# Performance work log

Hardware: AMD Instinct MI355X
Metric: run time of the kernel (lower is better)

## Reference

```python
import jax, jax.numpy as jnp
import numpy as np

D_K = 64
SCALE = 1.0 / np.sqrt(D_K).astype(np.float32)


def setup_inputs() -> dict:
    key = jax.random.key(0)
    kq, kk, kv = jax.random.split(key, 3)
    B, S, D = 4, 2048, 512
    q = jax.random.normal(kq, (B, S, D), dtype=jnp.float32)
    k = jax.random.normal(kk, (B, S, D), dtype=jnp.float32)
    v = jax.random.normal(kv, (B, S, D), dtype=jnp.float32)
    return {"q": q, "k": k, "v": v}


def reference(q, k, v):
    # n_head == 1: the per-head strided slices are the full tensors.
    # Original computes BOTH 'new_k' (scaled q@k^T) and 'new_v' (unscaled q@k^T);
    # note: v is never used in the original forward math (faithful reproduction).
    qk = jnp.einsum('bsd,btd->bst', q, k)           # [B, S, S]
    scores = qk * SCALE                              # new_k
    attn = jax.nn.softmax(scores, axis=2)            # softmax over dim 2
    # dropout with p=0.1 is identity in eval / deterministic reference
    out = jnp.matmul(attn, qk)                       # attn @ new_v -> [B, S, S]
    return out
```

## Files before the change

### kernel.cpp

```cpp
#include <hip/hip_runtime.h>
#include <hip/hip_bf16.h>
#include <stdint.h>


#define SS 2048
#define DD 512
#define BATCH 4
#define NT 32

typedef __attribute__((ext_vector_type(8))) short short8;
typedef __attribute__((ext_vector_type(8))) _Float16 half8;
typedef __attribute__((ext_vector_type(4))) float floatx4;
typedef __attribute__((ext_vector_type(4))) float float4v;
typedef __attribute__((ext_vector_type(4))) unsigned int uintx4;

#define GLOBAL_AS const __attribute__((address_space(1)))
#define LDS_AS __attribute__((address_space(3)))

__device__ __forceinline__ float bf2f(uint32_t hbits) {
    union { uint32_t u; float f; } c; c.u = hbits << 16; return c.f;
}
__device__ __forceinline__ uint32_t f2bf_rne(float f) {
    union { float f; uint32_t u; } c; c.f = f;
    return (c.u + 0x7fffu + ((c.u >> 16) & 1u)) >> 16;
}
__device__ __forceinline__ uint32_t pk2h(float x, float y) {
    _Float16 hx = (_Float16)x, hy = (_Float16)y;
    union { _Float16 h; uint16_t u; } cx, cy;
    cx.h = hx; cy.h = hy;
    return (uint32_t)cx.u | ((uint32_t)cy.u << 16);
}

union PackU { uint32_t u[4]; short8 s8; };

__global__ __launch_bounds__(256, 2) void gemm1_kernel(
    const float* __restrict__ Q, const float* __restrict__ K,
    uint16_t* __restrict__ qk, uint16_t* __restrict__ qkT)
{
    const int b  = blockIdx.z;
    const int s0 = blockIdx.y * 128;
    const int t0 = blockIdx.x * 128;
    const float* qb = Q + (size_t)b * SS * DD;
    const float* kb = K + (size_t)b * SS * DD;

    __shared__ uint16_t Ah[2 * 128 * 32];
    __shared__ uint16_t Bh[2 * 128 * 32];

    const int tid  = threadIdx.x;
    const int lane = tid & 63;
    const int wave = tid >> 6;
    const int wm   = wave >> 1;
    const int wn   = wave & 1;
    const int fm   = lane & 15;
    const int quad = lane >> 4;

    floatx4 acc[4][4];
#pragma unroll
    for (int i = 0; i < 4; ++i)
#pragma unroll
        for (int j = 0; j < 4; ++j)
            acc[i][j] = (floatx4)0.0f;

    const int r  = tid >> 1;
    const int c0 = (tid & 1) * 16;
    const float* gA = qb + (size_t)(s0 + r) * DD + c0;
    const float* gB = kb + (size_t)(t0 + r) * DD + c0;

    for (int k0 = 0; k0 < DD; k0 += 64) {
        uint32_t pa[2][8], pb[2][8];
#pragma unroll
        for (int ks = 0; ks < 2; ++ks) {
            float4v a4[4], b4[4];
#pragma unroll
            for (int l = 0; l < 4; ++l) {
                a4[l] = *(const float4v*)(gA + k0 + ks * 32 + l * 4);
                b4[l] = *(const float4v*)(gB + k0 + ks * 32 + l * 4);
            }
#pragma unroll
            for (int l = 0; l < 4; ++l) {
                pa[ks][2 * l]     = pk2h(a4[l][0], a4[l][1]);
                pa[ks][2 * l + 1] = pk2h(a4[l][2], a4[l][3]);
                pb[ks][2 * l]     = pk2h(b4[l][0], b4[l][1]);
                pb[ks][2 * l + 1] = pk2h(b4[l][2], b4[l][3]);
            }
        }
        __syncthreads();
#pragma unroll
        for (int ks = 0; ks < 2; ++ks) {
            PackU p;
            p.u[0]=pa[ks][0]; p.u[1]=pa[ks][1]; p.u[2]=pa[ks][2]; p.u[3]=pa[ks][3];
            *(short8*)(&Ah[ks * 4096 + r * 32 + c0]) = p.s8;
            p.u[0]=pa[ks][4]; p.u[1]=pa[ks][5]; p.u[2]=pa[ks][6]; p.u[3]=pa[ks][7];
            *(short8*)(&Ah[ks * 4096 + r * 32 + c0 + 8]) = p.s8;
            p.u[0]=pb[ks][0]; p.u[1]=pb[ks][1]; p.u[2]=pb[ks][2]; p.u[3]=pb[ks][3];
            *(short8*)(&Bh[ks * 4096 + r * 32 + c0]) = p.s8;
            p.u[0]=pb[ks][4]; p.u[1]=pb[ks][5]; p.u[2]=pb[ks][6]; p.u[7==7?7:7]=pb[ks][7];
            p.u[0]=pb[ks][4]; p.u[1]=pb[ks][5]; p.u[2]=pb[ks][6]; p.u[3]=pb[ks][7];
            *(short8*)(&Bh[ks * 4096 + r * 32 + c0 + 8]) = p.s8;
        }
        __syncthreads();

#pragma unroll
        for (int ks = 0; ks < 2; ++ks) {
            half8 fa[4], fb[4];
#pragma unroll
            for (int mt = 0; mt < 4; ++mt)
                fa[mt] = *(const half8*)(&Ah[ks * 4096 + (wm * 64 + mt * 16 + fm) * 32 + quad * 8]);
#pragma unroll
            for (int nt = 0; nt < 4; ++nt)
                fb[nt] = *(const half8*)(&Bh[ks * 4096 + (wn * 64 + nt * 16 + fm) * 32 + quad * 8]);
#pragma unroll
            for (int mt = 0; mt < 4; ++mt)
#pragma unroll
                for (int nt = 0; nt < 4; ++nt)
                    acc[mt][nt] = __builtin_amdgcn_mfma_f32_16x16x32_f16(fa[mt], fb[nt], acc[mt][nt], 0, 0, 0);
        }
    }

    uint16_t* qkb  = qk  + (size_t)b * SS * SS;
    uint16_t* qkTb = qkT + (size_t)b * SS * SS;
#pragma unroll
    for (int mt = 0; mt < 4; ++mt) {
#pragma unroll
        for (int nt = 0; nt < 4; ++nt) {
            const int srow = s0 + wm * 64 + mt * 16 + quad * 4;
            const int tcol = t0 + wn * 64 + nt * 16 + fm;
            uint32_t b0 = f2bf_rne(acc[mt][nt][0]);
            uint32_t b1 = f2bf_rne(acc[mt][nt][1]);
            uint32_t b2 = f2bf_rne(acc[mt][nt][2]);
            uint32_t b3 = f2bf_rne(acc[mt][nt][3]);
            qkb[(size_t)(srow + 0) * SS + tcol] = (uint16_t)b0;
            qkb[(size_t)(srow + 1) * SS + tcol] = (uint16_t)b1;
            qkb[(size_t)(srow + 2) * SS + tcol] = (uint16_t)b2;
            qkb[(size_t)(srow + 3) * SS + tcol] = (uint16_t)b3;
            uint2 pk = make_uint2(b0 | (b1 << 16), b2 | (b3 << 16));
            *(uint2*)(&qkTb[(size_t)tcol * SS + srow]) = pk;
        }
    }
}

__global__ __launch_bounds__(256) void softmax_inplace(uint16_t* __restrict__ qk)
{
    const size_t row = blockIdx.x;
    uint16_t* x = qk + row * SS;
    const int tid  = threadIdx.x;
    const int lane = tid & 63;
    const int wave = tid >> 6;

    uintx4 raw = *(const uintx4*)(x + tid * 8);
    float v[8];
#pragma unroll
    for (int i = 0; i < 4; ++i) {
        uint32_t u = raw[i];
        v[2 * i]     = bf2f(u & 0xffffu) * 0.125f;
        v[2 * i + 1] = bf2f(u >> 16) * 0.125f;
    }
    float m = v[0];
#pragma unroll
    for (int j = 1; j < 8; ++j) m = fmaxf(m, v[j]);
#pragma unroll
    for (int off = 1; off < 64; off <<= 1) m = fmaxf(m, __shfl_xor(m, off, 64));
    __shared__ float red[8];
    if (lane == 0) red[wave] = m;
    __syncthreads();
    m = fmaxf(fmaxf(red[0], red[1]), fmaxf(red[2], red[3]));

    float s = 0.f;
#pragma unroll
    for (int j = 0; j < 8; ++j) { v[j] = __expf(v[j] - m); s += v[j]; }
#pragma unroll
    for (int off = 1; off < 64; off <<= 1) s += __shfl_xor(s, off, 64);
    if (lane == 0) red[4 + wave] = s;
    __syncthreads();
    s = (red[4] + red[5]) + (red[6] + red[7]);
    const float inv = 1.0f / s;
#pragma unroll
    for (int i = 0; i < 4; ++i)
        raw[i] = f2bf_rne(v[2 * i] * inv) | (f2bf_rne(v[2 * i + 1] * inv) << 16);
    *(uintx4*)(x + tid * 8) = raw;
}

__global__ __launch_bounds__(512, 2) void gemm2_kernel(
    const uint16_t* __restrict__ attn, const uint16_t* __restrict__ qkT,
    float* __restrict__ out)
{
    const int b  = blockIdx.z;
    const int s0 = blockIdx.y * 256;
    const int t0 = blockIdx.x * 256;
    const uint16_t* ab = attn + (size_t)b * SS * SS;
    const uint16_t* bb = qkT  + (size_t)b * SS * SS;

    __shared__ uint16_t smem[65536];

    const int tid  = threadIdx.x;
    const int lane = tid & 63;
    const int wave = tid >> 6;
    const int wm   = wave >> 2;
    const int wn   = wave & 3;
    const int fm   = lane & 15;
    const int quad = lane >> 4;

    floatx4 acc[8][4];
#pragma unroll
    for (int i = 0; i < 8; ++i)
#pragma unroll
        for (int j = 0; j < 4; ++j)
            acc[i][j] = (floatx4)0.0f;

    const int sl0  = (quad ^ (fm & 7)) * 8;
    const int aoff = (wm * 128 + fm) * 64;
    const int boff = 32768 + (wn * 64 + fm) * 64;

    const int c0 = wave * 128 + lane;
    const int r0 = c0 >> 3;  const int l0 = ((c0 & 7) ^ (r0 & 7)) * 8;
    const int c1 = c0 + 64;
    const int r1 = c1 >> 3;  const int l1 = ((c1 & 7) ^ (r1 & 7)) * 8;
    const int ldsW = wave * 1024;

    auto STAGE_A = [&](int tt, int h) {
        uint16_t* base = &smem[(tt & 1) * 16384 + h * 8192 + ldsW];
        __builtin_amdgcn_global_load_lds(
            (GLOBAL_AS void*)(ab + (size_t)(s0 + h * 128 + r0) * SS + tt * 64 + l0),
            (LDS_AS void*)(base), 16, 0, 0);
        __builtin_amdgcn_global_load_lds(
            (GLOBAL_AS void*)(ab + (size_t)(s0 + h * 128 + r1) * SS + tt * 64 + l1),
            (LDS_AS void*)(base + 512), 16, 0, 0);
    };
    auto STAGE_B = [&](int tt, int h) {
        uint16_t* base = &smem[32768 + (tt & 1) * 16384 + h * 8192 + ldsW];
        __builtin_amdgcn_global_load_lds(
            (GLOBAL_AS void*)(bb + (size_t)(t0 + h * 128 + r0) * SS + tt * 64 + l0),
            (LDS_AS void*)(base), 16, 0, 0);
        __builtin_amdgcn_global_load_lds(
            (GLOBAL_AS void*)(bb + (size_t)(t0 + h * 128 + r1) * SS + tt * 64 + l1),
            (LDS_AS void*)(base + 512), 16, 0, 0);
    };

    STAGE_A(0, 0); STAGE_A(0, 1); STAGE_B(0, 0); STAGE_B(0, 1);
    STAGE_B(1, 0); STAGE_B(1, 1);
    asm volatile("s_waitcnt vmcnt(4)" ::: "memory");
    __builtin_amdgcn_s_barrier();

    short8 aF[4], aF2[4], bF[4][2];

    for (int t = 0; t < NT; ++t) {
        const int abase = (t & 1) * 16384;
        const int bbase = (t & 1) * 16384;

#pragma unroll
        for (int nt = 0; nt < 4; ++nt) {
            bF[nt][0] = *(const short8*)&smem[bbase + boff + nt * 1024 + sl0];
            bF[nt][1] = *(const short8*)&smem[bbase + boff + nt * 1024 + (sl0 ^ 32)];
        }
#pragma unroll
        for (int m = 0; m < 4; ++m)
            aF[m] = *(const short8*)&smem[abase + aoff + m * 1024 + sl0];
        if (t + 1 < NT) STAGE_A(t + 1, 0);
        __builtin_amdgcn_s_barrier();
        asm volatile("s_waitcnt lgkmcnt(0)" ::: "memory");
        __builtin_amdgcn_s_setprio(1);
#pragma unroll
        for (int m = 0; m < 4; ++m)
#pragma unroll
            for (int nt = 0; nt < 4; ++nt)
                acc[m][nt] = __builtin_amdgcn_mfma_f32_16x16x32_bf16(aF[m], bF[nt][0], acc[m][nt], 0, 0, 0);
        __builtin_amdgcn_s_setprio(0);
        __builtin_amdgcn_s_barrier();

#pragma unroll
        for (int m = 0; m < 4; ++m)
            aF2[m] = *(const short8*)&smem[abase + aoff + (m + 4) * 1024 + sl0];
        if (t + 1 < NT) STAGE_A(t + 1, 1);
        __builtin_amdgcn_s_barrier();
        asm volatile("s_waitcnt lgkmcnt(0)" ::: "memory");
        __builtin_amdgcn_s_setprio(1);
#pragma unroll
        for (int m = 0; m < 4; ++m)
#pragma unroll
            for (int nt = 0; nt < 4; ++nt)
                acc[m + 4][nt] = __builtin_amdgcn_mfma_f32_16x16x32_bf16(aF2[m], bF[nt][0], acc[m + 4][nt], 0, 0, 0);
        __builtin_amdgcn_s_setprio(0);
        __builtin_amdgcn_s_barrier();

#pragma unroll
        for (int m = 0; m < 4; ++m)
            aF[m] = *(const short8*)&smem[abase + aoff + m * 1024 + (sl0 ^ 32)];
        if (t + 2 < NT) STAGE_B(t + 2, 0);
        __builtin_amdgcn_s_barrier();
        asm volatile("s_waitcnt lgkmcnt(0)" ::: "memory");
        __builtin_amdgcn_s_setprio(1);
#pragma unroll
        for (int m = 0; m < 4; ++m)
#pragma unroll
            for (int nt = 0; nt < 4; ++nt)
                acc[m][nt] = __builtin_amdgcn_mfma_f32_16x16x32_bf16(aF[m], bF[nt][1], acc[m][nt], 0, 0, 0);
        __builtin_amdgcn_s_setprio(0);
        __builtin_amdgcn_s_barrier();

#pragma unroll
        for (int m = 0; m < 4; ++m)
            aF2[m] = *(const short8*)&smem[abase + aoff + (m + 4) * 1024 + (sl0 ^ 32)];
        if (t + 2 < NT) {
            STAGE_B(t + 2, 1);
            asm volatile("s_waitcnt vmcnt(4)" ::: "memory");
        } else {
            asm volatile("s_waitcnt vmcnt(0)" ::: "memory");
        }
        __builtin_amdgcn_s_barrier();
        asm volatile("s_waitcnt lgkmcnt(0)" ::: "memory");
        __builtin_amdgcn_s_setprio(1);
#pragma unroll
        for (int m = 0; m < 4; ++m)
#pragma unroll
            for (int nt = 0; nt < 4; ++nt)
                acc[m + 4][nt] = __builtin_amdgcn_mfma_f32_16x16x32_bf16(aF2[m], bF[nt][1], acc[m + 4][nt], 0, 0, 0);
        __builtin_amdgcn_s_setprio(0);
        __builtin_amdgcn_s_barrier();
    }

    float* ob = out + (size_t)b * SS * SS;
#pragma unroll
    for (int mt = 0; mt < 8; ++mt) {
#pragma unroll
        for (int nt = 0; nt < 4; ++nt) {
            const int srow = s0 + wm * 128 + mt * 16 + quad * 4;
            const int tcol = t0 + wn * 64 + nt * 16 + fm;
#pragma unroll
            for (int reg = 0; reg < 4; ++reg)
                ob[(size_t)(srow + reg) * SS + tcol] = acc[mt][nt][reg];
        }
    }
}

extern "C" void kernel_launch(void* const* d_in, const int* in_sizes, int n_in,
                              void* d_out, int out_size, void* d_ws, size_t ws_size,
                              hipStream_t stream) {
    const float* q = (const float*)d_in[0];
    const float* k = (const float*)d_in[1];
    float* out = (float*)d_out;

    uint16_t* qk  = (uint16_t*)d_ws;
    uint16_t* qkT = qk + (size_t)BATCH * SS * SS;

    dim3 grid1(SS / 128, SS / 128, BATCH);
    gemm1_kernel<<<grid1, 256, 0, stream>>>(q, k, qk, qkT);
    softmax_inplace<<<dim3(BATCH * SS), 256, 0, stream>>>(qk);
    dim3 grid2(SS / 256, SS / 256, BATCH);
    gemm2_kernel<<<grid2, 512, 0, stream>>>(qk, qkT, out);
}
```

Measured before the change: 228.7 us.

## Reassociate attn@(QK^T) as (attn@Q)@K^T to shrink second GEMM

Replaces the S×S×S second GEMM (attn @ qk) with two GEMMs, attn @ Q (S×S×D) followed by the result @ K^T (S×D×S), using associativity. This cuts the FLOPs of that stage by about 2x and removes the S×S transposed qk write from gemm1. It adds a prep kernel that casts Q (transposed) and K to bf16, plus an intermediate tmp buffer. Rounding to bf16 at different points changes the numerics slightly.

New measurement: 225.1 us. No clear change (-1.6%).

```diff
diff --git a/kernel.cpp b/kernel.cpp
--- a/kernel.cpp
+++ b/kernel.cpp
@@ -6,7 +6,7 @@
 #define SS 2048
 #define DD 512
 #define BATCH 4
-#define NT 32
+#define NTB 8
 
 typedef __attribute__((ext_vector_type(8))) short short8;
 typedef __attribute__((ext_vector_type(8))) _Float16 half8;
@@ -33,9 +33,79 @@
 
 union PackU { uint32_t u[4]; short8 s8; };
 
+__global__ __launch_bounds__(256) void prep_kernel(
+    const float* __restrict__ Q, const float* __restrict__ K,
+    uint16_t* __restrict__ qT, uint16_t* __restrict__ kB)
+{
+    const int b   = blockIdx.z;
+    const int tid = threadIdx.x;
+
+    if (blockIdx.y == 8) {
+        const float* kb_ = K + (size_t)b * SS * DD;
+        uint16_t* ob = kB + (size_t)b * SS * DD;
+        const int g0 = blockIdx.x * 256 + tid;
+#pragma unroll
+        for (int i = 0; i < 16; ++i) {
+            const int g = g0 + i * 8192;
+            const float4v* src = (const float4v*)(kb_ + (size_t)g * 8);
+            float4v x0 = src[0], x1 = src[1];
+            PackU p;
+            p.u[0] = f2bf_rne(x0[0]) | (f2bf_rne(x0[1]) << 16);
+            p.u[1] = f2bf_rne(x0[2]) | (f2bf_rne(x0[3]) << 16);
+            p.u[2] = f2bf_rne(x1[0]) | (f2bf_rne(x1[1]) << 16);
+            p.u[3] = f2bf_rne(x1[2]) | (f2bf_rne(x1[3]) << 16);
+            *(short8*)(ob + (size_t)g * 8) = p.s8;
+        }
+        return;
+    }
+
+    const int u0 = blockIdx.x * 64;
+    const int d0 = blockIdx.y * 64;
+    const float* qb = Q + (size_t)b * SS * DD;
+    uint16_t* qTb = qT + (size_t)b * DD * SS;
+
+    __shared__ uint16_t T[64 * 66];
+
+    {
+        const int r  = tid >> 2;
+        const int c4 = (tid & 3) * 16;
+        const float* src = qb + (size_t)(u0 + r) * DD + d0 + c4;
+        float4v x0 = *(const float4v*)(src + 0);
+        float4v x1 = *(const float4v*)(src + 4);
+        float4v x2 = *(const float4v*)(src + 8);
+        float4v x3 = *(const float4v*)(src + 12);
+        uint32_t w0 = f2bf_rne(x0[0]) | (f2bf_rne(x0[1]) << 16);
+        uint32_t w1 = f2bf_rne(x0[2]) | (f2bf_rne(x0[3]) << 16);
+        uint32_t w2 = f2bf_rne(x1[0]) | (f2bf_rne(x1[1]) << 16);
+        uint32_t w3 = f2bf_rne(x1[2]) | (f2bf_rne(x1[3]) << 16);
+        uint32_t w4 = f2bf_rne(x2[0]) | (f2bf_rne(x2[1]) << 16);
+        uint32_t w5 = f2bf_rne(x2[2]) | (f2bf_rne(x2[3]) << 16);
+        uint32_t w6 = f2bf_rne(x3[0]) | (f2bf_rne(x3[1]) << 16);
+        uint32_t w7 = f2bf_rne(x3[2]) | (f2bf_rne(x3[3]) << 16);
+        uint32_t* tw = (uint32_t*)&T[r * 66 + c4];
+        tw[0] = w0; tw[1] = w1; tw[2] = w2; tw[3] = w3;
+        tw[4] = w4; tw[5] = w5; tw[6] = w6; tw[7] = w7;
+    }
+    __syncthreads();
+#pragma unroll
+    for (int p = 0; p < 2; ++p) {
+        const int dl  = (tid >> 3) + p * 32;
+        const int ul8 = (tid & 7) * 8;
+        uint16_t t8[8];
+#pragma unroll
+        for (int j = 0; j < 8; ++j) t8[j] = T[(ul8 + j) * 66 + dl];
+        PackU o;
+        o.u[0] = (uint32_t)t8[0] | ((uint32_t)t8[1] << 16);
+        o.u[1] = (uint32_t)t8[2] | ((uint32_t)t8[3] << 16);
+        o.u[2] = (uint32_t)t8[4] | ((uint32_t)t8[5] << 16);
+        o.u[3] = (uint32_t)t8[6] | ((uint32_t)t8[7] << 16);
+        *(short8*)(&qTb[(size_t)(d0 + dl) * SS + u0 + ul8]) = o.s8;
+    }
+}
+
 __global__ __launch_bounds__(256, 2) void gemm1_kernel(
     const float* __restrict__ Q, const float* __restrict__ K,
-    uint16_t* __restrict__ qk, uint16_t* __restrict__ qkT)
+    uint16_t* __restrict__ qk)
 {
     const int b  = blockIdx.z;
     const int s0 = blockIdx.y * 128;
@@ -94,7 +164,6 @@
             *(short8*)(&Ah[ks * 4096 + r * 32 + c0 + 8]) = p.s8;
             p.u[0]=pb[ks][0]; p.u[1]=pb[ks][1]; p.u[2]=pb[ks][2]; p.u[3]=pb[ks][3];
             *(short8*)(&Bh[ks * 4096 + r * 32 + c0]) = p.s8;
-            p.u[0]=pb[ks][4]; p.u[1]=pb[ks][5]; p.u[2]=pb[ks][6]; p.u[7==7?7:7]=pb[ks][7];
             p.u[0]=pb[ks][4]; p.u[1]=pb[ks][5]; p.u[2]=pb[ks][6]; p.u[3]=pb[ks][7];
             *(short8*)(&Bh[ks * 4096 + r * 32 + c0 + 8]) = p.s8;
         }
@@ -117,24 +186,17 @@
         }
     }
 
-    uint16_t* qkb  = qk  + (size_t)b * SS * SS;
-    uint16_t* qkTb = qkT + (size_t)b * SS * SS;
+    uint16_t* qkb = qk + (size_t)b * SS * SS;
 #pragma unroll
     for (int mt = 0; mt < 4; ++mt) {
 #pragma unroll
         for (int nt = 0; nt < 4; ++nt) {
             const int srow = s0 + wm * 64 + mt * 16 + quad * 4;
             const int tcol = t0 + wn * 64 + nt * 16 + fm;
-            uint32_t b0 = f2bf_rne(acc[mt][nt][0]);
-            uint32_t b1 = f2bf_rne(acc[mt][nt][1]);
-            uint32_t b2 = f2bf_rne(acc[mt][nt][2]);
-            uint32_t b3 = f2bf_rne(acc[mt][nt][3]);
-            qkb[(size_t)(srow + 0) * SS + tcol] = (uint16_t)b0;
-            qkb[(size_t)(srow + 1) * SS + tcol] = (uint16_t)b1;
-            qkb[(size_t)(srow + 2) * SS + tcol] = (uint16_t)b2;
-            qkb[(size_t)(srow + 3) * SS + tcol] = (uint16_t)b3;
-            uint2 pk = make_uint2(b0 | (b1 << 16), b2 | (b3 << 16));
-            *(uint2*)(&qkTb[(size_t)tcol * SS + srow]) = pk;
+            qkb[(size_t)(srow + 0) * SS + tcol] = (uint16_t)f2bf_rne(acc[mt][nt][0]);
+            qkb[(size_t)(srow + 1) * SS + tcol] = (uint16_t)f2bf_rne(acc[mt][nt][1]);
+            qkb[(size_t)(srow + 2) * SS + tcol] = (uint16_t)f2bf_rne(acc[mt][nt][2]);
+            qkb[(size_t)(srow + 3) * SS + tcol] = (uint16_t)f2bf_rne(acc[mt][nt][3]);
         }
     }
 }
@@ -180,15 +242,101 @@
     *(uintx4*)(x + tid * 8) = raw;
 }
 
-__global__ __launch_bounds__(512, 2) void gemm2_kernel(
-    const uint16_t* __restrict__ attn, const uint16_t* __restrict__ qkT,
+__global__ __launch_bounds__(256, 2) void gemm2a_kernel(
+    const uint16_t* __restrict__ attn, const uint16_t* __restrict__ qT,
+    uint16_t* __restrict__ tmp)
+{
+    const int b  = blockIdx.z;
+    const int s0 = blockIdx.y * 128;
+    const int t0 = blockIdx.x * 128;
+    const uint16_t* ab = attn + (size_t)b * SS * SS;
+    const uint16_t* bb = qT   + (size_t)b * DD * SS;
+
+    __shared__ uint16_t As[2 * 128 * 32];
+    __shared__ uint16_t Bs[2 * 128 * 32];
+
+    const int tid  = threadIdx.x;
+    const int lane = tid & 63;
+    const int wave = tid >> 6;
+    const int wm = wave >> 1, wn = wave & 1;
+    const int fm = lane & 15, quad = lane >> 4;
+
+    floatx4 acc[4][4];
+#pragma unroll
+    for (int i = 0; i < 4; ++i)
+#pragma unroll
+        for (int j = 0; j < 4; ++j)
+            acc[i][j] = (floatx4)0.0f;
+
+    const int c0i = wave * 128 + lane;
+    const int c1i = c0i + 64;
+    const int rA0 = c0i >> 2, pA0 = c0i & 3;
+    const int rA1 = c1i >> 2, pA1 = c1i & 3;
+    const int ldsOff0 = (wave * 128) * 8;
+    const int ldsOff1 = (wave * 128 + 64) * 8;
+
+    for (int k0 = 0; k0 < SS; k0 += 64) {
+        __syncthreads();
+#pragma unroll
+        for (int ks = 0; ks < 2; ++ks) {
+            const int kc = k0 + ks * 32;
+            uint16_t* asub = &As[ks * 4096];
+            uint16_t* bsub = &Bs[ks * 4096];
+            __builtin_amdgcn_global_load_lds(
+                (GLOBAL_AS void*)(ab + (size_t)(s0 + rA0) * SS + kc + pA0 * 8),
+                (LDS_AS void*)(asub + ldsOff0), 16, 0, 0);
+            __builtin_amdgcn_global_load_lds(
+                (GLOBAL_AS void*)(ab + (size_t)(s0 + rA1) * SS + kc + pA1 * 8),
+                (LDS_AS void*)(asub + ldsOff1), 16, 0, 0);
+            __builtin_amdgcn_global_load_lds(
+                (GLOBAL_AS void*)(bb + (size_t)(t0 + rA0) * SS + kc + pA0 * 8),
+                (LDS_AS void*)(bsub + ldsOff0), 16, 0, 0);
+            __builtin_amdgcn_global_load_lds(
+                (GLOBAL_AS void*)(bb + (size_t)(t0 + rA1) * SS + kc + pA1 * 8),
+                (LDS_AS void*)(bsub + ldsOff1), 16, 0, 0);
+        }
+        __syncthreads();
+
+#pragma unroll
+        for (int ks = 0; ks < 2; ++ks) {
+            short8 fa[4], fb[4];
+#pragma unroll
+            for (int mt = 0; mt < 4; ++mt)
+                fa[mt] = *(const short8*)(&As[ks * 4096 + (wm * 64 + mt * 16 + fm) * 32 + quad * 8]);
+#pragma unroll
+            for (int nt = 0; nt < 4; ++nt)
+                fb[nt] = *(const short8*)(&Bs[ks * 4096 + (wn * 64 + nt * 16 + fm) * 32 + quad * 8]);
+#pragma unroll
+            for (int mt = 0; mt < 4; ++mt)
+#pragma unroll
+                for (int nt = 0; nt < 4; ++nt)
+                    acc[mt][nt] = __builtin_amdgcn_mfma_f32_16x16x32_bf16(fa[mt], fb[nt], acc[mt][nt], 0, 0, 0);
+        }
+    }
+
+    uint16_t* tb = tmp + (size_t)b * SS * DD;
+#pragma unroll
+    for (int mt = 0; mt < 4; ++mt) {
+#pragma unroll
+        for (int nt = 0; nt < 4; ++nt) {
+            const int srow = s0 + wm * 64 + mt * 16 + quad * 4;
+            const int tcol = t0 + wn * 64 + nt * 16 + fm;
+#pragma unroll
+            for (int reg = 0; reg < 4; ++reg)
+                tb[(size_t)(srow + reg) * DD + tcol] = (uint16_t)f2bf_rne(acc[mt][nt][reg]);
+        }
+    }
+}
+
+__global__ __launch_bounds__(512, 2) void gemm2b_kernel(
+    const uint16_t* __restrict__ tmp, const uint16_t* __restrict__ kB,
     float* __restrict__ out)
 {
     const int b  = blockIdx.z;
     const int s0 = blockIdx.y * 256;
     const int t0 = blockIdx.x * 256;
-    const uint16_t* ab = attn + (size_t)b * SS * SS;
-    const uint16_t* bb = qkT  + (size_t)b * SS * SS;
+    const uint16_t* ab = tmp + (size_t)b * SS * DD;
+    const uint16_t* bb = kB  + (size_t)b * SS * DD;
 
     __shared__ uint16_t smem[65536];
 
@@ -220,19 +368,19 @@
     auto STAGE_A = [&](int tt, int h) {
         uint16_t* base = &smem[(tt & 1) * 16384 + h * 8192 + ldsW];
         __builtin_amdgcn_global_load_lds(
-            (GLOBAL_AS void*)(ab + (size_t)(s0 + h * 128 + r0) * SS + tt * 64 + l0),
+            (GLOBAL_AS void*)(ab + (size_t)(s0 + h * 128 + r0) * DD + tt * 64 + l0),
             (LDS_AS void*)(base), 16, 0, 0);
         __builtin_amdgcn_global_load_lds(
-            (GLOBAL_AS void*)(ab + (size_t)(s0 + h * 128 + r1) * SS + tt * 64 + l1),
+            (GLOBAL_AS void*)(ab + (size_t)(s0 + h * 128 + r1) * DD + tt * 64 + l1),
             (LDS_AS void*)(base + 512), 16, 0, 0);
     };
     auto STAGE_B = [&](int tt, int h) {
         uint16_t* base = &smem[32768 + (tt & 1) * 16384 + h * 8192 + ldsW];
         __builtin_amdgcn_global_load_lds(
-            (GLOBAL_AS void*)(bb + (size_t)(t0 + h * 128 + r0) * SS + tt * 64 + l0),
+            (GLOBAL_AS void*)(bb + (size_t)(t0 + h * 128 + r0) * DD + tt * 64 + l0),
             (LDS_AS void*)(base), 16, 0, 0);
         __builtin_amdgcn_global_load_lds(
-            (GLOBAL_AS void*)(bb + (size_t)(t0 + h * 128 + r1) * SS + tt * 64 + l1),
+            (GLOBAL_AS void*)(bb + (size_t)(t0 + h * 128 + r1) * DD + tt * 64 + l1),
             (LDS_AS void*)(base + 512), 16, 0, 0);
     };
 
@@ -243,7 +391,7 @@
 
     short8 aF[4], aF2[4], bF[4][2];
 
-    for (int t = 0; t < NT; ++t) {
+    for (int t = 0; t < NTB; ++t) {
         const int abase = (t & 1) * 16384;
         const int bbase = (t & 1) * 16384;
 
@@ -255,7 +403,7 @@
 #pragma unroll
         for (int m = 0; m < 4; ++m)
             aF[m] = *(const short8*)&smem[abase + aoff + m * 1024 + sl0];
-        if (t + 1 < NT) STAGE_A(t + 1, 0);
+        if (t + 1 < NTB) STAGE_A(t + 1, 0);
         __builtin_amdgcn_s_barrier();
         asm volatile("s_waitcnt lgkmcnt(0)" ::: "memory");
         __builtin_amdgcn_s_setprio(1);
@@ -270,7 +418,7 @@
 #pragma unroll
         for (int m = 0; m < 4; ++m)
             aF2[m] = *(const short8*)&smem[abase + aoff + (m + 4) * 1024 + sl0];
-        if (t + 1 < NT) STAGE_A(t + 1, 1);
+        if (t + 1 < NTB) STAGE_A(t + 1, 1);
         __builtin_amdgcn_s_barrier();
         asm volatile("s_waitcnt lgkmcnt(0)" ::: "memory");
         __builtin_amdgcn_s_setprio(1);
@@ -285,7 +433,7 @@
 #pragma unroll
         for (int m = 0; m < 4; ++m)
             aF[m] = *(const short8*)&smem[abase + aoff + m * 1024 + (sl0 ^ 32)];
-        if (t + 2 < NT) STAGE_B(t + 2, 0);
+        if (t + 2 < NTB) STAGE_B(t + 2, 0);
         __builtin_amdgcn_s_barrier();
         asm volatile("s_waitcnt lgkmcnt(0)" ::: "memory");
         __builtin_amdgcn_s_setprio(1);
@@ -300,7 +448,7 @@
 #pragma unroll
         for (int m = 0; m < 4; ++m)
             aF2[m] = *(const short8*)&smem[abase + aoff + (m + 4) * 1024 + (sl0 ^ 32)];
-        if (t + 2 < NT) {
+        if (t + 2 < NTB) {
             STAGE_B(t + 2, 1);
             asm volatile("s_waitcnt vmcnt(4)" ::: "memory");
         } else {
@@ -340,11 +488,14 @@
     float* out = (float*)d_out;
 
     uint16_t* qk  = (uint16_t*)d_ws;
-    uint16_t* qkT = qk + (size_t)BATCH * SS * SS;
+    uint16_t* qT  = qk + (size_t)BATCH * SS * SS;
+    uint16_t* kB  = qT + (size_t)BATCH * DD * SS;
+    uint16_t* tmp = kB + (size_t)BATCH * SS * DD;
 
     dim3 grid1(SS / 128, SS / 128, BATCH);
-    gemm1_kernel<<<grid1, 256, 0, stream>>>(q, k, qk, qkT);
+    gemm1_kernel<<<grid1, 256, 0, stream>>>(q, k, qk);
+    prep_kernel<<<dim3(32, 9, BATCH), 256, 0, stream>>>(q, k, qT, kB);
     softmax_inplace<<<dim3(BATCH * SS), 256, 0, stream>>>(qk);
-    dim3 grid2(SS / 256, SS / 256, BATCH);
-    gemm2_kernel<<<grid2, 512, 0, stream>>>(qk, qkT, out);
-}
+    gemm2a_kernel<<<dim3(DD / 128, SS / 128, BATCH), 256, 0, stream>>>(qk, qT, tmp);
+    gemm2b_kernel<<<dim3(SS / 256, SS / 256, BATCH), 512, 0, stream>>>(tmp, kB, out);
+}
```
